# Kernel optimization log

Hardware: AMD Instinct MI355X
Metric: run time of the kernel (lower is better)

The kernel has to match this reference:

```python
import jax, jax.numpy as jnp
import numpy as np

# ---- hash-grid config (from module source) ----
L = 16          # n_levels
F = 2           # n_features_per_level
T = 1 << 19     # hashmap size
BASE = 16
SCALE = 1.3819
RES = [int(np.floor(BASE * SCALE ** l)) for l in range(L)]
DENSE = [(r + 1) ** 3 <= T for r in RES]   # levels 0-4 dense, rest hashed
PRIMES = np.array([1, 2654435761, 805459861], dtype=np.uint32)
OFFS = np.array([[i, j, k] for k in (0, 1) for j in (0, 1) for i in (0, 1)], dtype=np.float32)  # [8,3]
OFFS_U = OFFS.astype(np.uint32)


def hash_grid_encode(xyz, table):
    # xyz: [N,3] in [0,1); table: [L,T,F]
    feats = []
    for l in range(L):
        res = RES[l]
        pos = xyz * res                      # [N,3]
        p0f = jnp.floor(pos)
        w = pos - p0f                        # trilinear weights, [N,3]
        p0 = p0f.astype(jnp.uint32)          # [N,3]
        corner = p0[:, None, :] + OFFS_U[None]            # [N,8,3] uint32
        if DENSE[l]:
            s = np.uint32(res + 1)
            idx = corner[..., 0] + corner[..., 1] * s + corner[..., 2] * (s * s)
        else:
            idx = (corner[..., 0] * PRIMES[0]) ^ (corner[..., 1] * PRIMES[1]) ^ (corner[..., 2] * PRIMES[2])
            idx = idx % np.uint32(T)
        # corner weights: prod_d (offs ? w : 1-w)  -> [N,8]
        wts = jnp.prod(jnp.where(OFFS[None].astype(bool), w[:, None, :], 1.0 - w[:, None, :]), axis=-1)
        f = table[l][idx]                    # gather: [N,8,F]
        feats.append(jnp.sum(f * wts[..., None], axis=1))  # [N,F]
    return jnp.concatenate(feats, axis=-1)   # [N, L*F=32]


def sh_deg4(d):
    # d in [-1,1]^3; returns [N,16] real SH basis (tcnn ordering/constants)
    x, y, z = d[:, 0], d[:, 1], d[:, 2]
    x2, y2, z2 = x * x, y * y, z * z
    xy, yz, xz = x * y, y * z, x * z
    return jnp.stack([
        jnp.full_like(x, 0.28209479177387814),
        -0.48860251190291987 * y,
        0.48860251190291987 * z,
        -0.48860251190291987 * x,
        1.0925484305920792 * xy,
        -1.0925484305920792 * yz,
        0.94617469575755997 * z2 - 0.31539156525251999,
        -1.0925484305920792 * xz,
        0.54627421529603959 * (x2 - y2),
        0.59004358992664352 * y * (-3.0 * x2 + y2),
        2.8906114426405538 * xy * z,
        0.45704579946446572 * y * (1.0 - 5.0 * z2),
        0.3731763325901154 * z * (5.0 * z2 - 3.0),
        0.45704579946446572 * x * (1.0 - 5.0 * z2),
        1.4453057213202769 * z * (x2 - y2),
        0.59004358992664352 * x * (-x2 + 3.0 * y2),
    ], axis=-1)


def setup_inputs() -> dict:
    key = jax.random.key(0)
    ks = jax.random.split(key, 8)
    N = 2 ** 21
    xyz = jax.random.uniform(ks[0], (N, 3), dtype=jnp.float32)
    dir = jax.random.uniform(ks[1], (N, 3), dtype=jnp.float32)
    # hash table init per tcnn: uniform in [-1e-4, 1e-4]
    hash_table = jax.random.uniform(ks[2], (L, T, F), dtype=jnp.float32, minval=-1e-4, maxval=1e-4)
    def he(k, fan_in, shape):
        return jax.random.normal(k, shape, dtype=jnp.float32) * np.sqrt(2.0 / fan_in)
    w_sigma1 = he(ks[3], 32, (32, 64))
    w_sigma2 = he(ks[4], 64, (64, 17))   # 1 + geo_feat_dim(16)
    w_rgb1 = he(ks[5], 32, (32, 64))     # 16 (SH) + 16 (geo)
    w_rgb2 = he(ks[6], 64, (64, 64))
    w_rgb3 = he(ks[7], 64, (64, 3))
    return {"xyz": xyz, "dir": dir, "hash_table": hash_table,
            "w_sigma1": w_sigma1, "w_sigma2": w_sigma2,
            "w_rgb1": w_rgb1, "w_rgb2": w_rgb2, "w_rgb3": w_rgb3}


def reference(xyz, dir, hash_table, w_sigma1, w_sigma2, w_rgb1, w_rgb2, w_rgb3):
    xyz_flat = xyz.reshape(-1, 3)
    dir_flat = dir.reshape(-1, 3)
    enc = hash_grid_encode(xyz_flat, hash_table)                 # [N,32]
    h = jax.nn.relu(enc @ w_sigma1)
    geometry = h @ w_sigma2                                       # [N,17]
    sigma, geo_feat = geometry[..., :1], geometry[..., 1:]
    dir_enc = sh_deg4(dir_flat * 2.0 - 1.0)                       # [N,16]
    rgb_in = jnp.concatenate([dir_enc, geo_feat], axis=-1)        # [N,32]
    h = jax.nn.relu(rgb_in @ w_rgb1)
    h = jax.nn.relu(h @ w_rgb2)
    rgb = h @ w_rgb3                                              # [N,3]
    rgb_unflat = rgb.reshape(xyz.shape)
    sigma_unflat = sigma.reshape(xyz.shape[:-1] + (1,))
    return jax.nn.sigmoid(rgb_unflat), jax.nn.relu(sigma_unflat)
```

## Files before the change

### kernel.cpp

```cpp
#include <hip/hip_runtime.h>
#include <hip/hip_bf16.h>
#include <cmath>

#define TBL (1 << 19)

__device__ __forceinline__ float relu_f(float x) { return fmaxf(x, 0.0f); }

__device__ __forceinline__ unsigned short f2bf(float x) {
    union { float f; unsigned u; } v; v.f = x;
    const unsigned r = v.u + 0x7FFFu + ((v.u >> 16) & 1u);
    return (unsigned short)(r >> 16);
}

typedef __attribute__((ext_vector_type(8))) short short8;
typedef __attribute__((ext_vector_type(4))) float floatx4;

#define RES_LIST {16, 22, 30, 42, 58, 80, 111, 153, 212, 294, 406, 561, 775, 1072, 1481, 2047}

__global__ __launch_bounds__(256, 8)
void encode_sched(const float* __restrict__ xyz,
                  const float* __restrict__ table,
                  unsigned* __restrict__ ws_enc,
                  int n)
{
    constexpr unsigned RES[16] = RES_LIST;
    constexpr unsigned LEVP[8] = {0x00665555u, 0x00777766u, 0x11998888u, 0x11AAAA99u,
                                  0x222CBBBBu, 0x332DDCCCu, 0x433EEEDDu, 0x444FFFFEu};
    constexpr unsigned QTRP[8] = {0x44E4u, 0xEE4Eu, 0x44E4u, 0xEE4Eu,
                                  0x90E4u, 0x4D39u, 0x3A4Eu, 0xE793u};

    const int xcd      = (int)(blockIdx.x & 7u);
    const unsigned g   = blockIdx.x >> 3;
    const unsigned upb = (unsigned)(n >> 10);
    const int unit     = (int)(g / upb);
    const int slot     = (int)(g % upb);
    const int level    = (int)((LEVP[xcd] >> (4 * unit)) & 15u);
    const int quarter  = (int)((QTRP[xcd] >> (2 * unit)) & 3u);
    const int i        = quarter * (n >> 2) + slot * 256 + (int)threadIdx.x;
    if (i >= n) return;

    const float px_ = __builtin_nontemporal_load(xyz + 3 * (size_t)i + 0);
    const float py_ = __builtin_nontemporal_load(xyz + 3 * (size_t)i + 1);
    const float pz_ = __builtin_nontemporal_load(xyz + 3 * (size_t)i + 2);

    const unsigned res = RES[level];
    const float fr = (float)res;
    const float posx = px_ * fr, posy = py_ * fr, posz = pz_ * fr;
    const float fx = floorf(posx), fy = floorf(posy), fz = floorf(posz);
    const float wx = posx - fx, wy = posy - fy, wz = posz - fz;
    const unsigned x0 = (unsigned)fx, y0 = (unsigned)fy, z0 = (unsigned)fz;
    const float* tb = table + (size_t)level * (TBL * 2);

    float a0 = 0.0f, a1 = 0.0f;
    const float wx1 = wx, wx0 = 1.0f - wx;

    if (level < 5) {
        const unsigned s = res + 1u;
        const unsigned s2 = s * s;
        const unsigned base = x0 + y0 * s + z0 * s2;
#pragma unroll
        for (int c = 0; c < 4; ++c) {
            const unsigned dy = c & 1, dz = c >> 1;
            const unsigned idx = base + dy * s + dz * s2;
            const float wyz = (dy ? wy : 1.0f - wy) * (dz ? wz : 1.0f - wz);
            const float w0 = wyz * wx0, w1 = wyz * wx1;
            float e0x, e0y, e1x, e1y;
            if (!(idx & 1u)) {
                const float4 f = *reinterpret_cast<const float4*>(tb + 2u * idx);
                e0x = f.x; e0y = f.y; e1x = f.z; e1y = f.w;
            } else {
                const float2 f0 = *reinterpret_cast<const float2*>(tb + 2u * idx);
                const float2 f1 = *reinterpret_cast<const float2*>(tb + 2u * idx + 2u);
                e0x = f0.x; e0y = f0.y; e1x = f1.x; e1y = f1.y;
            }
            a0 = fmaf(e0x, w0, fmaf(e1x, w1, a0));
            a1 = fmaf(e0y, w0, fmaf(e1y, w1, a1));
        }
    } else {
#pragma unroll
        for (int c = 0; c < 4; ++c) {
            const unsigned dy = c & 1, dz = c >> 1;
            const unsigned hh = (y0 + dy) * 2654435761u ^ (z0 + dz) * 805459861u;
            const float wyz = (dy ? wy : 1.0f - wy) * (dz ? wz : 1.0f - wz);
            const float w0 = wyz * wx0, w1 = wyz * wx1;
            const unsigned i0 = (x0 ^ hh) & (unsigned)(TBL - 1);
            if (!(x0 & 1u)) {
                const float4 f = *reinterpret_cast<const float4*>(tb + 2u * (i0 & ~1u));
                const bool hi = (i0 & 1u) != 0u;
                const float e0x = hi ? f.z : f.x, e0y = hi ? f.w : f.y;
                const float e1x = hi ? f.x : f.z, e1y = hi ? f.y : f.w;
                a0 = fmaf(e0x, w0, fmaf(e1x, w1, a0));
                a1 = fmaf(e0y, w0, fmaf(e1y, w1, a1));
            } else {
                const unsigned i1 = ((x0 + 1u) ^ hh) & (unsigned)(TBL - 1);
                const float2 f0 = *reinterpret_cast<const float2*>(tb + 2u * i0);
                const float2 f1 = *reinterpret_cast<const float2*>(tb + 2u * i1);
                a0 = fmaf(f0.x, w0, fmaf(f1.x, w1, a0));
                a1 = fmaf(f0.y, w0, fmaf(f1.y, w1, a1));
            }
        }
    }

    const unsigned pack = (unsigned)f2bf(a0) | ((unsigned)f2bf(a1) << 16);
    __builtin_nontemporal_store(pack, ws_enc + ((size_t)level * n + i));
}

__global__ __launch_bounds__(256)
void mlp_mfma(const unsigned* __restrict__ ws_enc,
              const float* __restrict__ dirv,
              const float* __restrict__ ws1,
              const float* __restrict__ ws2,
              const float* __restrict__ wr1,
              const float* __restrict__ wr2,
              const float* __restrict__ wr3,
              float* __restrict__ out,
              int n)
{
    __shared__ alignas(16) unsigned short s_w[13184];
    __shared__ alignas(16) unsigned short s_act[4 * 16 * 72];
    __shared__ alignas(16) float          s_geo[4 * 16 * 20];

    const int tid = threadIdx.x;

    for (int e = tid; e < 13184; e += 256) s_w[e] = 0;
    __syncthreads();
    for (int e = tid; e < 2048; e += 256) { const int k = e >> 6, j = e & 63; s_w[0     + j * 40 + k] = f2bf(ws1[e]); }
    for (int e = tid; e < 1088; e += 256) { const int k = e / 17, j = e % 17; s_w[2560  + j * 72 + k] = f2bf(ws2[e]); }
    for (int e = tid; e < 2048; e += 256) { const int k = e >> 6, j = e & 63; s_w[4864  + j * 40 + k] = f2bf(wr1[e]); }
    for (int e = tid; e < 4096; e += 256) { const int k = e >> 6, j = e & 63; s_w[7424  + j * 72 + k] = f2bf(wr2[e]); }
    for (int e = tid; e < 192;  e += 256) { const int k = e / 3,  j = e % 3;  s_w[12032 + j * 72 + k] = f2bf(wr3[e]); }
    __syncthreads();

    const int wave = tid >> 6;
    const int lane = tid & 63;
    const int q    = lane >> 4;
    const int mr   = lane & 15;
    unsigned short* hb = s_act + wave * (16 * 72);
    float*          gb = s_geo + wave * (16 * 20);
    const int base = blockIdx.x * 256 + wave * 64;
    if (base >= n) return;

#pragma unroll 1
    for (int mt = 0; mt < 4; ++mt) {
        const int pt = base + mt * 16 + mr;

        short8 aenc;
#pragma unroll
        for (int t = 0; t < 4; ++t) {
            const unsigned e = ws_enc[(size_t)(q * 4 + t) * n + pt];
            aenc[2 * t + 0] = (short)(e & 0xFFFFu);
            aenc[2 * t + 1] = (short)(e >> 16);
        }

#pragma unroll
        for (int nc = 0; nc < 4; ++nc) {
            const short8 b = *reinterpret_cast<const short8*>(s_w + 0 + (nc * 16 + mr) * 40 + q * 8);
            floatx4 acc = {0.f, 0.f, 0.f, 0.f};
            acc = __builtin_amdgcn_mfma_f32_16x16x32_bf16(aenc, b, acc, 0, 0, 0);
#pragma unroll
            for (int r = 0; r < 4; ++r)
                hb[(q * 4 + r) * 72 + nc * 16 + mr] = f2bf(fmaxf(acc[r], 0.f));
        }
        __builtin_amdgcn_wave_barrier();

        {
            const short8 a0 = *reinterpret_cast<const short8*>(hb + mr * 72 + 0  + q * 8);
            const short8 a1 = *reinterpret_cast<const short8*>(hb + mr * 72 + 32 + q * 8);
            floatx4 acc0 = {0.f, 0.f, 0.f, 0.f};
            floatx4 acc1 = {0.f, 0.f, 0.f, 0.f};
            {
                const short8 b0 = *reinterpret_cast<const short8*>(s_w + 2560 + mr * 72 + 0  + q * 8);
                const short8 b1 = *reinterpret_cast<const short8*>(s_w + 2560 + mr * 72 + 32 + q * 8);
                acc0 = __builtin_amdgcn_mfma_f32_16x16x32_bf16(a0, b0, acc0, 0, 0, 0);
                acc0 = __builtin_amdgcn_mfma_f32_16x16x32_bf16(a1, b1, acc0, 0, 0, 0);
            }
            {
                const short8 b0 = *reinterpret_cast<const short8*>(s_w + 2560 + (16 + mr) * 72 + 0  + q * 8);
                const short8 b1 = *reinterpret_cast<const short8*>(s_w + 2560 + (16 + mr) * 72 + 32 + q * 8);
                acc1 = __builtin_amdgcn_mfma_f32_16x16x32_bf16(a0, b0, acc1, 0, 0, 0);
                acc1 = __builtin_amdgcn_mfma_f32_16x16x32_bf16(a1, b1, acc1, 0, 0, 0);
            }
#pragma unroll
            for (int r = 0; r < 4; ++r) gb[(q * 4 + r) * 20 + mr + 3] = acc0[r];
            if (mr == 0) {
#pragma unroll
                for (int r = 0; r < 4; ++r) gb[(q * 4 + r) * 20 + 19] = acc1[r];
            }
        }
        __builtin_amdgcn_wave_barrier();

        if (lane < 16)
            out[3 * (size_t)n + (size_t)(base + mt * 16 + lane)] = fmaxf(gb[lane * 20 + 3], 0.f);

        const float dx = dirv[3 * (size_t)pt + 0] * 2.0f - 1.0f;
        const float dy = dirv[3 * (size_t)pt + 1] * 2.0f - 1.0f;
        const float dz = dirv[3 * (size_t)pt + 2] * 2.0f - 1.0f;
        const float x2 = dx * dx, y2 = dy * dy, z2 = dz * dz;
        const float xy = dx * dy, yz = dy * dz, xz = dx * dz;
        float sh[16];
        sh[0]  = 0.28209479177387814f;
        sh[1]  = -0.48860251190291987f * dy;
        sh[2]  = 0.48860251190291987f * dz;
        sh[3]  = -0.48860251190291987f * dx;
        sh[4]  = 1.0925484305920792f * xy;
        sh[5]  = -1.0925484305920792f * yz;
        sh[6]  = 0.94617469575756f * z2 - 0.31539156525252f;
        sh[7]  = -1.0925484305920792f * xz;
        sh[8]  = 0.5462742152960396f * (x2 - y2);
        sh[9]  = 0.5900435899266435f * dy * (-3.0f * x2 + y2);
        sh[10] = 2.890611442640554f * xy * dz;
        sh[11] = 0.4570457994644657f * dy * (1.0f - 5.0f * z2);
        sh[12] = 0.3731763325901154f * dz * (5.0f * z2 - 3.0f);
        sh[13] = 0.4570457994644657f * dx * (1.0f - 5.0f * z2);
        sh[14] = 1.445305721320277f * dz * (x2 - y2);
        sh[15] = 0.5900435899266435f * dx * (-x2 + 3.0f * y2);

        short8 ar;
        if (q < 2) {
#pragma unroll
            for (int j = 0; j < 8; ++j) ar[j] = (short)f2bf(sh[q * 8 + j]);
        } else {
            const floatx4 g0 = *reinterpret_cast<const floatx4*>(gb + mr * 20 + 4 + (q - 2) * 8);
            const floatx4 g1 = *reinterpret_cast<const floatx4*>(gb + mr * 20 + 8 + (q - 2) * 8);
#pragma unroll
            for (int j = 0; j < 4; ++j) { ar[j] = (short)f2bf(g0[j]); ar[4 + j] = (short)f2bf(g1[j]); }
        }

#pragma unroll
        for (int nc = 0; nc < 4; ++nc) {
            const short8 b = *reinterpret_cast<const short8*>(s_w + 4864 + (nc * 16 + mr) * 40 + q * 8);
            floatx4 acc = {0.f, 0.f, 0.f, 0.f};
            acc = __builtin_amdgcn_mfma_f32_16x16x32_bf16(ar, b, acc, 0, 0, 0);
#pragma unroll
            for (int r = 0; r < 4; ++r)
                hb[(q * 4 + r) * 72 + nc * 16 + mr] = f2bf(fmaxf(acc[r], 0.f));
        }
        __builtin_amdgcn_wave_barrier();

        {
            const short8 a0 = *reinterpret_cast<const short8*>(hb + mr * 72 + 0  + q * 8);
            const short8 a1 = *reinterpret_cast<const short8*>(hb + mr * 72 + 32 + q * 8);
            __builtin_amdgcn_wave_barrier();
#pragma unroll
            for (int nc = 0; nc < 4; ++nc) {
                const short8 b0 = *reinterpret_cast<const short8*>(s_w + 7424 + (nc * 16 + mr) * 72 + 0  + q * 8);
                const short8 b1 = *reinterpret_cast<const short8*>(s_w + 7424 + (nc * 16 + mr) * 72 + 32 + q * 8);
                floatx4 acc = {0.f, 0.f, 0.f, 0.f};
                acc = __builtin_amdgcn_mfma_f32_16x16x32_bf16(a0, b0, acc, 0, 0, 0);
                acc = __builtin_amdgcn_mfma_f32_16x16x32_bf16(a1, b1, acc, 0, 0, 0);
#pragma unroll
                for (int r = 0; r < 4; ++r)
                    hb[(q * 4 + r) * 72 + nc * 16 + mr] = f2bf(fmaxf(acc[r], 0.f));
            }
        }
        __builtin_amdgcn_wave_barrier();

        {
            const short8 a0 = *reinterpret_cast<const short8*>(hb + mr * 72 + 0  + q * 8);
            const short8 a1 = *reinterpret_cast<const short8*>(hb + mr * 72 + 32 + q * 8);
            const short8 b0 = *reinterpret_cast<const short8*>(s_w + 12032 + mr * 72 + 0  + q * 8);
            const short8 b1 = *reinterpret_cast<const short8*>(s_w + 12032 + mr * 72 + 32 + q * 8);
            floatx4 acc = {0.f, 0.f, 0.f, 0.f};
            acc = __builtin_amdgcn_mfma_f32_16x16x32_bf16(a0, b0, acc, 0, 0, 0);
            acc = __builtin_amdgcn_mfma_f32_16x16x32_bf16(a1, b1, acc, 0, 0, 0);
            if (mr < 3) {
#pragma unroll
                for (int r = 0; r < 4; ++r) {
                    const int p = base + mt * 16 + q * 4 + r;
                    out[3 * (size_t)p + mr] = 1.0f / (1.0f + __expf(-acc[r]));
                }
            }
        }
        __builtin_amdgcn_wave_barrier();
    }
}

__global__ __launch_bounds__(256, 4)
void nerf_fused(const float* __restrict__ xyz,
                const float* __restrict__ dirv,
                const float* __restrict__ table,
                const float* __restrict__ ws1,
                const float* __restrict__ ws2,
                const float* __restrict__ wr1,
                const float* __restrict__ wr2,
                const float* __restrict__ wr3,
                float* __restrict__ out,
                int n)
{
    constexpr unsigned RES[16] = RES_LIST;

    const int i = blockIdx.x * 256 + threadIdx.x;
    if (i >= n) return;

    const float px_ = xyz[3 * (size_t)i + 0];
    const float py_ = xyz[3 * (size_t)i + 1];
    const float pz_ = xyz[3 * (size_t)i + 2];

    float enc[32];
#pragma unroll
    for (int l = 0; l < 16; ++l) {
        const unsigned res = RES[l];
        const float fr = (float)res;
        const float posx = px_ * fr, posy = py_ * fr, posz = pz_ * fr;
        const float fx = floorf(posx), fy = floorf(posy), fz = floorf(posz);
        const float wx = posx - fx, wy = posy - fy, wz = posz - fz;
        const unsigned x0 = (unsigned)fx, y0 = (unsigned)fy, z0 = (unsigned)fz;
        const float* tb = table + (size_t)l * (TBL * 2);
        float a0 = 0.0f, a1 = 0.0f;
#pragma unroll
        for (int c = 0; c < 8; ++c) {
            const unsigned cx = x0 + (c & 1);
            const unsigned cy = y0 + ((c >> 1) & 1);
            const unsigned cz = z0 + ((c >> 2) & 1);
            unsigned idx;
            if (l < 5) {
                const unsigned s = res + 1u;
                idx = cx + cy * s + cz * (s * s);
            } else {
                idx = (cx * 1u) ^ (cy * 2654435761u) ^ (cz * 805459861u);
                idx &= (unsigned)(TBL - 1);
            }
            const float w = ((c & 1) ? wx : 1.0f - wx) *
                            ((c & 2) ? wy : 1.0f - wy) *
                            ((c & 4) ? wz : 1.0f - wz);
            const float2 f = *reinterpret_cast<const float2*>(tb + 2u * idx);
            a0 = fmaf(f.x, w, a0);
            a1 = fmaf(f.y, w, a1);
        }
        enc[2 * l + 0] = a0;
        enc[2 * l + 1] = a1;
    }

    float h[64];
#pragma unroll
    for (int j = 0; j < 64; ++j) h[j] = 0.0f;
#pragma unroll
    for (int k = 0; k < 32; ++k) {
        const float e = enc[k];
#pragma unroll
        for (int j = 0; j < 64; ++j) h[j] = fmaf(e, ws1[k * 64 + j], h[j]);
    }
#pragma unroll
    for (int j = 0; j < 64; ++j) h[j] = relu_f(h[j]);

    float geo[17];
#pragma unroll
    for (int j = 0; j < 17; ++j) geo[j] = 0.0f;
#pragma unroll
    for (int k = 0; k < 64; ++k) {
        const float e = h[k];
#pragma unroll
        for (int j = 0; j < 17; ++j) geo[j] = fmaf(e, ws2[k * 17 + j], geo[j]);
    }
    out[3 * (size_t)n + (size_t)i] = relu_f(geo[0]);

    const float dx = dirv[3 * (size_t)i + 0] * 2.0f - 1.0f;
    const float dy = dirv[3 * (size_t)i + 1] * 2.0f - 1.0f;
    const float dz = dirv[3 * (size_t)i + 2] * 2.0f - 1.0f;
    const float x2 = dx * dx, y2 = dy * dy, z2 = dz * dz;
    const float xy = dx * dy, yz = dy * dz, xz = dx * dz;

    float sh[16];
    sh[0]  = 0.28209479177387814f;
    sh[1]  = -0.48860251190291987f * dy;
    sh[2]  = 0.48860251190291987f * dz;
    sh[3]  = -0.48860251190291987f * dx;
    sh[4]  = 1.0925484305920792f * xy;
    sh[5]  = -1.0925484305920792f * yz;
    sh[6]  = 0.94617469575756f * z2 - 0.31539156525252f;
    sh[7]  = -1.0925484305920792f * xz;
    sh[8]  = 0.5462742152960396f * (x2 - y2);
    sh[9]  = 0.5900435899266435f * dy * (-3.0f * x2 + y2);
    sh[10] = 2.890611442640554f * xy * dz;
    sh[11] = 0.4570457994644657f * dy * (1.0f - 5.0f * z2);
    sh[12] = 0.3731763325901154f * dz * (5.0f * z2 - 3.0f);
    sh[13] = 0.4570457994644657f * dx * (1.0f - 5.0f * z2);
    sh[14] = 1.445305721320277f * dz * (x2 - y2);
    sh[15] = 0.5900435899266435f * dx * (-x2 + 3.0f * y2);

    float g[64];
#pragma unroll
    for (int j = 0; j < 64; ++j) g[j] = 0.0f;
#pragma unroll
    for (int k = 0; k < 16; ++k) {
        const float e = sh[k];
#pragma unroll
        for (int j = 0; j < 64; ++j) g[j] = fmaf(e, wr1[k * 64 + j], g[j]);
    }
#pragma unroll
    for (int k = 16; k < 32; ++k) {
        const float e = geo[k - 15];
#pragma unroll
        for (int j = 0; j < 64; ++j) g[j] = fmaf(e, wr1[k * 64 + j], g[j]);
    }
#pragma unroll
    for (int j = 0; j < 64; ++j) g[j] = relu_f(g[j]);

    float r0 = 0.0f, r1 = 0.0f, r2 = 0.0f;
#pragma unroll
    for (int half = 0; half < 2; ++half) {
        const int j0 = half * 32;
        float g2h[32];
#pragma unroll
        for (int j = 0; j < 32; ++j) g2h[j] = 0.0f;
#pragma unroll
        for (int k = 0; k < 64; ++k) {
            const float e = g[k];
#pragma unroll
            for (int j = 0; j < 32; ++j) g2h[j] = fmaf(e, wr2[k * 64 + j0 + j], g2h[j]);
        }
#pragma unroll
        for (int j = 0; j < 32; ++j) {
            const float e = relu_f(g2h[j]);
            r0 = fmaf(e, wr3[(j0 + j) * 3 + 0], r0);
            r1 = fmaf(e, wr3[(j0 + j) * 3 + 1], r1);
            r2 = fmaf(e, wr3[(j0 + j) * 3 + 2], r2);
        }
    }

    out[3 * (size_t)i + 0] = 1.0f / (1.0f + __expf(-r0));
    out[3 * (size_t)i + 1] = 1.0f / (1.0f + __expf(-r1));
    out[3 * (size_t)i + 2] = 1.0f / (1.0f + __expf(-r2));
}

extern "C" void kernel_launch(void* const* d_in, const int* in_sizes, int n_in,
                              void* d_out, int out_size, void* d_ws, size_t ws_size,
                              hipStream_t stream)
{
    const float* xyz   = (const float*)d_in[0];
    const float* dirv  = (const float*)d_in[1];
    const float* table = (const float*)d_in[2];
    const float* ws1   = (const float*)d_in[3];
    const float* ws2   = (const float*)d_in[4];
    const float* wr1   = (const float*)d_in[5];
    const float* wr2   = (const float*)d_in[6];
    const float* wr3   = (const float*)d_in[7];
    float* out = (float*)d_out;

    const int n = in_sizes[0] / 3;
    const int blocks_per_level = (n + 255) / 256;
    dim3 block(256);
    dim3 grid_mlp(blocks_per_level);

    const size_t enc_bytes = (size_t)n * 16 * sizeof(unsigned);
    if (ws_size >= enc_bytes && n >= 1024 && (n & 1023) == 0) {
        unsigned* ws_enc = (unsigned*)d_ws;
        dim3 grid_enc(8u * 8u * (unsigned)(n >> 10));
        hipLaunchKernelGGL(encode_sched, grid_enc, block, 0, stream,
                           xyz, table, ws_enc, n);
        hipLaunchKernelGGL(mlp_mfma, grid_mlp, block, 0, stream,
                           ws_enc, dirv, ws1, ws2, wr1, wr2, wr3, out, n);
    } else {
        hipLaunchKernelGGL(nerf_fused, grid_mlp, block, 0, stream,
                           xyz, dirv, table, ws1, ws2, wr1, wr2, wr3, out, n);
    }
}
```

Before: 1.014 ms.

## Reschedule encode blocks per XCD by point slice and prefetch MLP inputs

The encode kernel's block-to-(level, point range) mapping changes from packed per-XCD level/quarter tables to a scheme where each XCD owns one eighth of the points and walks all 16 levels in an interleaved dense/hashed order. The aim is to keep each XCD's xyz slice in its own cache and balance hashed and dense levels over time. The MLP kernel now software-prefetches the next tile's encoded features and directions into registers and gets a launch-bounds occupancy hint. Risks are that the level tables no longer stay local to one XCD's L2, and that the added registers may lower occupancy.

```diff
diff --git a/kernel.cpp b/kernel.cpp
--- a/kernel.cpp
+++ b/kernel.cpp
@@ -24,19 +24,15 @@
                   int n)
 {
     constexpr unsigned RES[16] = RES_LIST;
-    constexpr unsigned LEVP[8] = {0x00665555u, 0x00777766u, 0x11998888u, 0x11AAAA99u,
-                                  0x222CBBBBu, 0x332DDCCCu, 0x433EEEDDu, 0x444FFFFEu};
-    constexpr unsigned QTRP[8] = {0x44E4u, 0xEE4Eu, 0x44E4u, 0xEE4Eu,
-                                  0x90E4u, 0x4D39u, 0x3A4Eu, 0xE793u};
+    constexpr int LEVORD[16] = {5, 0, 6, 1, 7, 2, 8, 3, 9, 4, 10, 11, 12, 13, 14, 15};
 
     const int xcd      = (int)(blockIdx.x & 7u);
     const unsigned g   = blockIdx.x >> 3;
-    const unsigned upb = (unsigned)(n >> 10);
+    const unsigned upb = (unsigned)(n >> 11);
     const int unit     = (int)(g / upb);
     const int slot     = (int)(g % upb);
-    const int level    = (int)((LEVP[xcd] >> (4 * unit)) & 15u);
-    const int quarter  = (int)((QTRP[xcd] >> (2 * unit)) & 3u);
-    const int i        = quarter * (n >> 2) + slot * 256 + (int)threadIdx.x;
+    const int level    = LEVORD[unit & 15];
+    const int i        = xcd * (n >> 3) + slot * 256 + (int)threadIdx.x;
     if (i >= n) return;
 
     const float px_ = __builtin_nontemporal_load(xyz + 3 * (size_t)i + 0);
@@ -105,7 +101,7 @@
     __builtin_nontemporal_store(pack, ws_enc + ((size_t)level * n + i));
 }
 
-__global__ __launch_bounds__(256)
+__global__ __launch_bounds__(256, 2)
 void mlp_mfma(const unsigned* __restrict__ ws_enc,
               const float* __restrict__ dirv,
               const float* __restrict__ ws1,
@@ -140,17 +136,35 @@
     const int base = blockIdx.x * 256 + wave * 64;
     if (base >= n) return;
 
+    const int pt0 = base + mr;
+    unsigned e0 = ws_enc[(size_t)(q * 4 + 0) * n + pt0];
+    unsigned e1 = ws_enc[(size_t)(q * 4 + 1) * n + pt0];
+    unsigned e2 = ws_enc[(size_t)(q * 4 + 2) * n + pt0];
+    unsigned e3 = ws_enc[(size_t)(q * 4 + 3) * n + pt0];
+    float dv0 = dirv[3 * (size_t)pt0 + 0];
+    float dv1 = dirv[3 * (size_t)pt0 + 1];
+    float dv2 = dirv[3 * (size_t)pt0 + 2];
+
 #pragma unroll 1
     for (int mt = 0; mt < 4; ++mt) {
-        const int pt = base + mt * 16 + mr;
+        unsigned f0 = 0, f1 = 0, f2 = 0, f3 = 0;
+        float c0 = 0.f, c1 = 0.f, c2 = 0.f;
+        if (mt < 3) {
+            const int ptn = pt0 + (mt + 1) * 16;
+            f0 = ws_enc[(size_t)(q * 4 + 0) * n + ptn];
+            f1 = ws_enc[(size_t)(q * 4 + 1) * n + ptn];
+            f2 = ws_enc[(size_t)(q * 4 + 2) * n + ptn];
+            f3 = ws_enc[(size_t)(q * 4 + 3) * n + ptn];
+            c0 = dirv[3 * (size_t)ptn + 0];
+            c1 = dirv[3 * (size_t)ptn + 1];
+            c2 = dirv[3 * (size_t)ptn + 2];
+        }
 
         short8 aenc;
-#pragma unroll
-        for (int t = 0; t < 4; ++t) {
-            const unsigned e = ws_enc[(size_t)(q * 4 + t) * n + pt];
-            aenc[2 * t + 0] = (short)(e & 0xFFFFu);
-            aenc[2 * t + 1] = (short)(e >> 16);
-        }
+        aenc[0] = (short)(e0 & 0xFFFFu); aenc[1] = (short)(e0 >> 16);
+        aenc[2] = (short)(e1 & 0xFFFFu); aenc[3] = (short)(e1 >> 16);
+        aenc[4] = (short)(e2 & 0xFFFFu); aenc[5] = (short)(e2 >> 16);
+        aenc[6] = (short)(e3 & 0xFFFFu); aenc[7] = (short)(e3 >> 16);
 
 #pragma unroll
         for (int nc = 0; nc < 4; ++nc) {
@@ -192,9 +206,9 @@
         if (lane < 16)
             out[3 * (size_t)n + (size_t)(base + mt * 16 + lane)] = fmaxf(gb[lane * 20 + 3], 0.f);
 
-        const float dx = dirv[3 * (size_t)pt + 0] * 2.0f - 1.0f;
-        const float dy = dirv[3 * (size_t)pt + 1] * 2.0f - 1.0f;
-        const float dz = dirv[3 * (size_t)pt + 2] * 2.0f - 1.0f;
+        const float dx = dv0 * 2.0f - 1.0f;
+        const float dy = dv1 * 2.0f - 1.0f;
+        const float dz = dv2 * 2.0f - 1.0f;
         const float x2 = dx * dx, y2 = dy * dy, z2 = dz * dz;
         const float xy = dx * dy, yz = dy * dz, xz = dx * dz;
         float sh[16];
@@ -272,6 +286,9 @@
             }
         }
         __builtin_amdgcn_wave_barrier();
+
+        e0 = f0; e1 = f1; e2 = f2; e3 = f3;
+        dv0 = c0; dv1 = c1; dv2 = c2;
     }
 }
 
@@ -443,9 +460,9 @@
     dim3 grid_mlp(blocks_per_level);
 
     const size_t enc_bytes = (size_t)n * 16 * sizeof(unsigned);
-    if (ws_size >= enc_bytes && n >= 1024 && (n & 1023) == 0) {
+    if (ws_size >= enc_bytes && n >= 2048 && (n & 2047) == 0) {
         unsigned* ws_enc = (unsigned*)d_ws;
-        dim3 grid_enc(8u * 8u * (unsigned)(n >> 10));
+        dim3 grid_enc(8u * 16u * (unsigned)(n >> 11));
         hipLaunchKernelGGL(encode_sched, grid_enc, block, 0, stream,
                            xyz, table, ws_enc, n);
         hipLaunchKernelGGL(mlp_mfma, grid_mlp, block, 0, stream,
```

Result: faster. 982.2 us (-3.2%).
